# Performance work log

Measured on AMD Instinct MI355X. Metric: run time of the kernel, lower is better.

Reference implementation:

```python
import jax, jax.numpy as jnp
import numpy as np

N_NODES = 100000

def setup_inputs() -> dict:
    key = jax.random.key(0)
    k1, k2, k3, k4, k5 = jax.random.split(key, 5)
    E = 1600000
    feat = jax.random.normal(k1, (N_NODES, 128), dtype=jnp.float32)
    W = jax.random.normal(k2, (128, 32), dtype=jnp.float32) * 0.08  # ~xavier scale
    edge_w = jax.random.uniform(k3, (E,), dtype=jnp.float32)
    src = jax.random.randint(k4, (E,), 0, N_NODES, dtype=jnp.int32)
    dst = jax.random.randint(k5, (E,), 0, N_NODES, dtype=jnp.int32)
    return {"feat": feat, "W": W, "edge_w": edge_w, "src": src, "dst": dst}

def reference(feat, W, edge_w, src, dst):
    # linear transform: [N, in] @ [in, out] -> [N, out]
    h = feat @ W
    # gather source features per edge, scale by edge weight: u_mul_e
    m = h[src] * edge_w[:, None]  # [E, out]
    # sum messages at destination nodes
    rst = jax.ops.segment_sum(m, dst, num_segments=N_NODES)  # [N, out]
    return rst
```

## Files before the change

### kernel.cpp

```cpp
#include <hip/hip_runtime.h>
#include <hip/hip_fp16.h>

constexpr int N_IN    = 128;
constexpr int N_OUT   = 32;
constexpr int LOG_R   = 6;
constexpr int RANGE   = 1 << LOG_R;
constexpr int MAXNB   = 2048;
constexpr int NCC     = 256;
constexpr int PBLK    = 512;
constexpr int CHUNK_P = 2048;

union H4 { uint2 u; __half2 h2[2]; };

__global__ __launch_bounds__(256) void gemm_h(
    const float* __restrict__ feat, const float* __restrict__ W,
    __half* __restrict__ h, int n)
{
    __shared__ float Ws[N_IN * N_OUT];
    for (int i = threadIdx.x; i < (N_IN * N_OUT) / 4; i += 256)
        reinterpret_cast<float4*>(Ws)[i] = reinterpret_cast<const float4*>(W)[i];
    __syncthreads();

    int gid = blockIdx.x * 256 + threadIdx.x;
    int row = gid >> 3;
    if (row >= n) return;
    int cg = (gid & 7) * 4;

    const float4* frow = reinterpret_cast<const float4*>(feat + (size_t)row * N_IN);
    float4 acc = make_float4(0.f, 0.f, 0.f, 0.f);
    #pragma unroll
    for (int k4 = 0; k4 < N_IN / 4; ++k4) {
        float4 f = frow[k4];
        int k = k4 * 4;
        float4 w0 = *reinterpret_cast<const float4*>(&Ws[(k + 0) * N_OUT + cg]);
        float4 w1 = *reinterpret_cast<const float4*>(&Ws[(k + 1) * N_OUT + cg]);
        float4 w2 = *reinterpret_cast<const float4*>(&Ws[(k + 2) * N_OUT + cg]);
        float4 w3 = *reinterpret_cast<const float4*>(&Ws[(k + 3) * N_OUT + cg]);
        acc.x += f.x * w0.x + f.y * w1.x + f.z * w2.x + f.w * w3.x;
        acc.y += f.x * w0.y + f.y * w1.y + f.z * w2.y + f.w * w3.y;
        acc.z += f.x * w0.z + f.y * w1.z + f.z * w2.z + f.w * w3.z;
        acc.w += f.x * w0.w + f.y * w1.w + f.z * w2.w + f.w * w3.w;
    }
    H4 v;
    v.h2[0] = __float22half2_rn(make_float2(acc.x, acc.y));
    v.h2[1] = __float22half2_rn(make_float2(acc.z, acc.w));
    *reinterpret_cast<uint2*>(h + (size_t)row * N_OUT + cg) = v.u;
}

__global__ __launch_bounds__(PBLK) void partition2_k(
    const int* __restrict__ src, const int* __restrict__ dst,
    const float* __restrict__ w, int* __restrict__ tbl,
    int2* __restrict__ sw, int E, int NB, int epc)
{
    __shared__ int hist[MAXNB];
    __shared__ int wscan[PBLK];

    const int c   = blockIdx.x;
    const int tid = threadIdx.x;
    const int e0  = c * epc;
    const int e1  = min(e0 + epc, E);
    const int m   = max(e1 - e0, 0);
    const int m4  = m & ~3;
    const int slots = (NB + PBLK - 1) / PBLK;

    for (int i = tid; i < NB; i += PBLK) hist[i] = 0;
    __syncthreads();

    for (int o = tid * 4; o < m4; o += PBLK * 4) {
        int4 dv = *reinterpret_cast<const int4*>(dst + e0 + o);
        atomicAdd(&hist[dv.x >> LOG_R], 1);
        atomicAdd(&hist[dv.y >> LOG_R], 1);
        atomicAdd(&hist[dv.z >> LOG_R], 1);
        atomicAdd(&hist[dv.w >> LOG_R], 1);
    }
    if (m4 + tid < m) atomicAdd(&hist[dst[e0 + m4 + tid] >> LOG_R], 1);
    __syncthreads();

    int tsum = 0;
    int base = tid * slots;
    for (int j = 0; j < slots; ++j) {
        int idx = base + j;
        if (idx < NB) tsum += hist[idx];
    }
    wscan[tid] = tsum;
    __syncthreads();
    for (int off = 1; off < PBLK; off <<= 1) {
        int x = (tid >= off) ? wscan[tid - off] : 0;
        __syncthreads();
        wscan[tid] += x;
        __syncthreads();
    }
    int run = wscan[tid] - tsum;
    __syncthreads();
    for (int j = 0; j < slots; ++j) {
        int idx = base + j;
        if (idx < NB) {
            int cval = hist[idx];
            tbl[(size_t)c * (NB + 1) + idx] = run;
            hist[idx] = run;
            run += cval;
        }
    }
    if (tid == 0) tbl[(size_t)c * (NB + 1) + NB] = m;
    __syncthreads();

    int2* outp = sw + (size_t)c * epc;
    for (int o = tid * 4; o < m4; o += PBLK * 4) {
        int4   sv = *reinterpret_cast<const int4*>(src + e0 + o);
        int4   dv = *reinterpret_cast<const int4*>(dst + e0 + o);
        float4 wv = *reinterpret_cast<const float4*>(w + e0 + o);
        int p0 = atomicAdd(&hist[dv.x >> LOG_R], 1);
        int p1 = atomicAdd(&hist[dv.y >> LOG_R], 1);
        int p2 = atomicAdd(&hist[dv.z >> LOG_R], 1);
        int p3 = atomicAdd(&hist[dv.w >> LOG_R], 1);
        outp[p0] = make_int2(sv.x | ((dv.x & (RANGE - 1)) << 17), __float_as_int(wv.x));
        outp[p1] = make_int2(sv.y | ((dv.y & (RANGE - 1)) << 17), __float_as_int(wv.y));
        outp[p2] = make_int2(sv.z | ((dv.z & (RANGE - 1)) << 17), __float_as_int(wv.z));
        outp[p3] = make_int2(sv.w | ((dv.w & (RANGE - 1)) << 17), __float_as_int(wv.w));
    }
    if (m4 + tid < m) {
        int e = e0 + m4 + tid;
        int d = dst[e];
        int pos = atomicAdd(&hist[d >> LOG_R], 1);
        outp[pos] = make_int2(src[e] | ((d & (RANGE - 1)) << 17), __float_as_int(w[e]));
    }
}

__global__ __launch_bounds__(256) void conv4_k(
    const __half* __restrict__ h, const int2* __restrict__ sw,
    const int* __restrict__ tbl, float* __restrict__ out,
    int n, int NB, int ncc, int epc)
{
    __shared__ int2 pairs[CHUNK_P];
    __shared__ int2 pairs_s[CHUNK_P];
    __shared__ int cnt[RANGE];
    __shared__ int sc[RANGE];
    __shared__ int start[RANGE + 1];
    __shared__ int cur[RANGE];
    __shared__ int rs[NCC];
    __shared__ int ps[NCC + 1];
    __shared__ int stmp[256];

    const int b   = blockIdx.x;
    const int tid = threadIdx.x;
    const int g   = tid >> 3;
    const int cg  = (tid & 7) * 4;

    int len = 0;
    if (tid < ncc) {
        int s0 = tbl[(size_t)tid * (NB + 1) + b];
        int s1 = tbl[(size_t)tid * (NB + 1) + b + 1];
        rs[tid] = s0;
        len = s1 - s0;
    }
    stmp[tid] = len;
    __syncthreads();
    for (int off = 1; off < 256; off <<= 1) {
        int x = (tid >= off) ? stmp[tid - off] : 0;
        __syncthreads();
        stmp[tid] += x;
        __syncthreads();
    }
    ps[tid + 1] = stmp[tid];
    if (tid == 0) ps[0] = 0;
    __syncthreads();
    const int deg = ps[ncc];

    float4 accA = make_float4(0.f, 0.f, 0.f, 0.f);
    float4 accB = make_float4(0.f, 0.f, 0.f, 0.f);

    #define LOAD_H(p, f01, f23)                                                \
        H4 _u##f01;                                                            \
        _u##f01.u = *reinterpret_cast<const uint2*>(                           \
            h + (size_t)((p).x & 0x1FFFF) * N_OUT + cg);                       \
        float2 f01 = __half22float2(_u##f01.h2[0]);                            \
        float2 f23 = __half22float2(_u##f01.h2[1]);
    #define ACC_STEP(p, f01, f23)                                              \
    {                                                                          \
        float wv  = __int_as_float((p).y);                                     \
        int   odd = ((p).x >> 17) & 1;                                         \
        float wa = odd ? 0.f : wv, wb = odd ? wv : 0.f;                        \
        accA.x += f01.x * wa; accA.y += f01.y * wa;                            \
        accA.z += f23.x * wa; accA.w += f23.y * wa;                            \
        accB.x += f01.x * wb; accB.y += f01.y * wb;                            \
        accB.z += f23.x * wb; accB.w += f23.y * wb;                            \
    }

    if (deg <= CHUNK_P) {
        if (tid < RANGE) cnt[tid] = 0;
        __syncthreads();

        if (tid < ncc) {
            int d0 = ps[tid];
            int l  = ps[tid + 1] - d0;
            const int2* sp = sw + (size_t)tid * epc + rs[tid];
            for (int j = 0; j < l; ++j) {
                int2 p = sp[j];
                pairs[d0 + j] = p;
                atomicAdd(&cnt[p.x >> 17], 1);
            }
        }
        __syncthreads();

        int v = 0;
        if (tid < RANGE) { v = cnt[tid]; sc[tid] = v; }
        __syncthreads();
        #pragma unroll
        for (int off = 1; off < RANGE; off <<= 1) {
            int x = (tid < RANGE && tid >= off) ? sc[tid - off] : 0;
            __syncthreads();
            if (tid < RANGE) sc[tid] += x;
            __syncthreads();
        }
        if (tid < RANGE) { start[tid] = sc[tid] - v; cur[tid] = sc[tid] - v; }
        if (tid == RANGE - 1) start[RANGE] = sc[RANGE - 1];
        __syncthreads();

        for (int i = tid; i < deg; i += 256) {
            int2 p = pairs[i];
            int pos = atomicAdd(&cur[p.x >> 17], 1);
            pairs_s[pos] = p;
        }
        __syncthreads();

        int k  = start[2 * g];
        int ke = start[2 * g + 2];
        for (; k + 3 < ke; k += 4) {
            int2 p0 = pairs_s[k + 0], p1 = pairs_s[k + 1];
            int2 p2 = pairs_s[k + 2], p3 = pairs_s[k + 3];
            LOAD_H(p0, a01, a23)
            LOAD_H(p1, b01, b23)
            LOAD_H(p2, c01, c23)
            LOAD_H(p3, d01, d23)
            ACC_STEP(p0, a01, a23)
            ACC_STEP(p1, b01, b23)
            ACC_STEP(p2, c01, c23)
            ACC_STEP(p3, d01, d23)
        }
        for (; k < ke; ++k) {
            int2 p = pairs_s[k];
            LOAD_H(p, e01, e23)
            ACC_STEP(p, e01, e23)
        }
    } else {
        for (int cbase = 0; cbase < deg; cbase += CHUNK_P) {
            const int m = min(CHUNK_P, deg - cbase);

            for (int i = tid; i < m; i += 256) {
                int gidx = cbase + i;
                int lo = 0, hi = ncc - 1;
                while (lo < hi) {
                    int mid = (lo + hi + 1) >> 1;
                    if (ps[mid] <= gidx) lo = mid; else hi = mid - 1;
                }
                int off = gidx - ps[lo];
                pairs[i] = sw[(size_t)lo * epc + rs[lo] + off];
            }
            if (tid < RANGE) cnt[tid] = 0;
            __syncthreads();

            for (int i = tid; i < m; i += 256)
                atomicAdd(&cnt[pairs[i].x >> 17], 1);
            __syncthreads();

            int v = 0;
            if (tid < RANGE) { v = cnt[tid]; sc[tid] = v; }
            __syncthreads();
            #pragma unroll
            for (int off = 1; off < RANGE; off <<= 1) {
                int x = (tid < RANGE && tid >= off) ? sc[tid - off] : 0;
                __syncthreads();
                if (tid < RANGE) sc[tid] += x;
                __syncthreads();
            }
            if (tid < RANGE) { start[tid] = sc[tid] - v; cur[tid] = sc[tid] - v; }
            if (tid == RANGE - 1) start[RANGE] = sc[RANGE - 1];
            __syncthreads();

            for (int i = tid; i < m; i += 256) {
                int2 p = pairs[i];
                int pos = atomicAdd(&cur[p.x >> 17], 1);
                pairs_s[pos] = p;
            }
            __syncthreads();

            int k  = start[2 * g];
            int ke = start[2 * g + 2];
            for (; k < ke; ++k) {
                int2 p = pairs_s[k];
                LOAD_H(p, f01, f23)
                ACC_STEP(p, f01, f23)
            }
            __syncthreads();
        }
    }
    #undef LOAD_H
    #undef ACC_STEP

    const int lo2 = b * RANGE;
    int node0 = lo2 + 2 * g;
    if (node0 < n)
        *reinterpret_cast<float4*>(out + (size_t)node0 * N_OUT + cg) = accA;
    if (node0 + 1 < n)
        *reinterpret_cast<float4*>(out + (size_t)(node0 + 1) * N_OUT + cg) = accB;
}

__global__ __launch_bounds__(256) void fused_edge(
    const float* __restrict__ feat, const float* __restrict__ W,
    const float* __restrict__ edge_w, const int* __restrict__ src,
    const int* __restrict__ dst, float* __restrict__ out, int E)
{
    __shared__ float Ws[N_IN * N_OUT];
    for (int i = threadIdx.x; i < (N_IN * N_OUT) / 4; i += 256)
        reinterpret_cast<float4*>(Ws)[i] = reinterpret_cast<const float4*>(W)[i];
    __syncthreads();
    int gid = blockIdx.x * 256 + threadIdx.x;
    int e = gid >> 3;
    if (e >= E) return;
    int cg = (gid & 7) * 4;
    int s = src[e];
    int d = dst[e];
    float w = edge_w[e];
    const float4* frow = reinterpret_cast<const float4*>(feat + (size_t)s * N_IN);
    float4 acc = make_float4(0.f, 0.f, 0.f, 0.f);
    #pragma unroll
    for (int k4 = 0; k4 < N_IN / 4; ++k4) {
        float4 f = frow[k4];
        int k = k4 * 4;
        float4 w0 = *reinterpret_cast<const float4*>(&Ws[(k + 0) * N_OUT + cg]);
        float4 w1 = *reinterpret_cast<const float4*>(&Ws[(k + 1) * N_OUT + cg]);
        float4 w2 = *reinterpret_cast<const float4*>(&Ws[(k + 2) * N_OUT + cg]);
        float4 w3 = *reinterpret_cast<const float4*>(&Ws[(k + 3) * N_OUT + cg]);
        acc.x += f.x * w0.x + f.y * w1.x + f.z * w2.x + f.w * w3.x;
        acc.y += f.x * w0.y + f.y * w1.y + f.z * w2.y + f.w * w3.y;
        acc.z += f.x * w0.z + f.y * w1.z + f.z * w2.z + f.w * w3.z;
        acc.w += f.x * w0.w + f.y * w1.w + f.z * w2.w + f.w * w3.w;
    }
    float* o = out + (size_t)d * N_OUT + cg;
    atomicAdd(o + 0, acc.x * w);
    atomicAdd(o + 1, acc.y * w);
    atomicAdd(o + 2, acc.z * w);
    atomicAdd(o + 3, acc.w * w);
}

extern "C" void kernel_launch(void* const* d_in, const int* in_sizes, int n_in,
                              void* d_out, int out_size, void* d_ws, size_t ws_size,
                              hipStream_t stream) {
    const float* feat   = (const float*)d_in[0];
    const float* W      = (const float*)d_in[1];
    const float* edge_w = (const float*)d_in[2];
    const int*   src    = (const int*)d_in[3];
    const int*   dst    = (const int*)d_in[4];
    float* out = (float*)d_out;

    int n = in_sizes[0] / N_IN;
    int E = in_sizes[2];

    int NB  = (n + RANGE - 1) / RANGE;
    int ncc = NCC;
    int epc = (((E + ncc - 1) / ncc) + 3) & ~3;

    size_t off_h   = 0;
    size_t off_tbl = (off_h + (size_t)n * N_OUT * sizeof(__half) + 15) & ~(size_t)15;
    size_t off_sw  = (off_tbl + (size_t)ncc * (NB + 1) * sizeof(int) + 15) & ~(size_t)15;
    size_t need    = off_sw + (size_t)ncc * epc * sizeof(int2);

    bool ok = (ws_size >= need) && (n <= (1 << 17)) && (NB <= MAXNB);

    if (ok) {
        char* ws = (char*)d_ws;
        __half* h  = (__half*)(ws + off_h);
        int*   tbl = (int*)(ws + off_tbl);
        int2*  sw  = (int2*)(ws + off_sw);

        long gthreads = (long)n * 8;
        gemm_h<<<(int)((gthreads + 255) / 256), 256, 0, stream>>>(feat, W, h, n);
        partition2_k<<<ncc, PBLK, 0, stream>>>(src, dst, edge_w, tbl, sw, E, NB, epc);
        conv4_k<<<NB, 256, 0, stream>>>(h, sw, tbl, out, n, NB, ncc, epc);
    } else {
        hipError_t _e = hipMemsetAsync(d_out, 0, (size_t)out_size * sizeof(float), stream);
        (void)_e;
        long sthreads = (long)E * 8;
        fused_edge<<<(int)((sthreads + 255) / 256), 256, 0, stream>>>(feat, W, edge_w, src, dst, out, E);
    }
}
```

Before: 78.65 us.

## Map four threads per node with 16-byte gathers and drop staging buffer

The aggregation kernel now gives each destination node four threads, each loading eight half values with one 16-byte load. Previously eight threads handled a pair of nodes and masked the weight to zero for the non-matching node. The intermediate shared pairs buffer is removed: each thread reads its chunk directly from global memory twice, once to histogram and once to scatter. The overflow path now has every thread scan the whole chunk and keep only its own node's edges, replacing the sort. This removes the wasted multiply-adds and a shared-memory copy, at the cost of re-reading global pairs and a slower fallback for high-degree blocks.

```diff
diff --git a/kernel.cpp b/kernel.cpp
--- a/kernel.cpp
+++ b/kernel.cpp
@@ -11,6 +11,7 @@
 constexpr int CHUNK_P = 2048;
 
 union H4 { uint2 u; __half2 h2[2]; };
+union H8 { uint4 u; __half2 h2[4]; };
 
 __global__ __launch_bounds__(256) void gemm_h(
     const float* __restrict__ feat, const float* __restrict__ W,
@@ -126,12 +127,11 @@
     }
 }
 
-__global__ __launch_bounds__(256) void conv4_k(
+__global__ __launch_bounds__(256) void conv5_k(
     const __half* __restrict__ h, const int2* __restrict__ sw,
     const int* __restrict__ tbl, float* __restrict__ out,
     int n, int NB, int ncc, int epc)
 {
-    __shared__ int2 pairs[CHUNK_P];
     __shared__ int2 pairs_s[CHUNK_P];
     __shared__ int cnt[RANGE];
     __shared__ int sc[RANGE];
@@ -141,10 +141,10 @@
     __shared__ int ps[NCC + 1];
     __shared__ int stmp[256];
 
-    const int b   = blockIdx.x;
-    const int tid = threadIdx.x;
-    const int g   = tid >> 3;
-    const int cg  = (tid & 7) * 4;
+    const int b    = blockIdx.x;
+    const int tid  = threadIdx.x;
+    const int node = tid >> 2;
+    const int cg8  = (tid & 3) * 8;
 
     int len = 0;
     if (tid < ncc) {
@@ -166,40 +166,35 @@
     __syncthreads();
     const int deg = ps[ncc];
 
-    float4 accA = make_float4(0.f, 0.f, 0.f, 0.f);
-    float4 accB = make_float4(0.f, 0.f, 0.f, 0.f);
-
-    #define LOAD_H(p, f01, f23)                                                \
-        H4 _u##f01;                                                            \
-        _u##f01.u = *reinterpret_cast<const uint2*>(                           \
-            h + (size_t)((p).x & 0x1FFFF) * N_OUT + cg);                       \
-        float2 f01 = __half22float2(_u##f01.h2[0]);                            \
-        float2 f23 = __half22float2(_u##f01.h2[1]);
-    #define ACC_STEP(p, f01, f23)                                              \
+    float4 acc01 = make_float4(0.f, 0.f, 0.f, 0.f);
+    float4 acc23 = make_float4(0.f, 0.f, 0.f, 0.f);
+
+    #define GLOAD(p, f0, f1, f2, f3)                                           \
+        H8 _x##f0;                                                             \
+        _x##f0.u = *reinterpret_cast<const uint4*>(                            \
+            h + (size_t)((p).x & 0x1FFFF) * N_OUT + cg8);                      \
+        float2 f0 = __half22float2(_x##f0.h2[0]);                              \
+        float2 f1 = __half22float2(_x##f0.h2[1]);                              \
+        float2 f2 = __half22float2(_x##f0.h2[2]);                              \
+        float2 f3 = __half22float2(_x##f0.h2[3]);
+    #define GACC(p, f0, f1, f2, f3)                                            \
     {                                                                          \
-        float wv  = __int_as_float((p).y);                                     \
-        int   odd = ((p).x >> 17) & 1;                                         \
-        float wa = odd ? 0.f : wv, wb = odd ? wv : 0.f;                        \
-        accA.x += f01.x * wa; accA.y += f01.y * wa;                            \
-        accA.z += f23.x * wa; accA.w += f23.y * wa;                            \
-        accB.x += f01.x * wb; accB.y += f01.y * wb;                            \
-        accB.z += f23.x * wb; accB.w += f23.y * wb;                            \
+        float wv = __int_as_float((p).y);                                      \
+        acc01.x += f0.x * wv; acc01.y += f0.y * wv;                            \
+        acc01.z += f1.x * wv; acc01.w += f1.y * wv;                            \
+        acc23.x += f2.x * wv; acc23.y += f2.y * wv;                            \
+        acc23.z += f3.x * wv; acc23.w += f3.y * wv;                            \
     }
 
     if (deg <= CHUNK_P) {
-        if (tid < RANGE) cnt[tid] = 0;
-        __syncthreads();
-
-        if (tid < ncc) {
-            int d0 = ps[tid];
-            int l  = ps[tid + 1] - d0;
-            const int2* sp = sw + (size_t)tid * epc + rs[tid];
-            for (int j = 0; j < l; ++j) {
-                int2 p = sp[j];
-                pairs[d0 + j] = p;
-                atomicAdd(&cnt[p.x >> 17], 1);
-            }
-        }
+        if (tid < RANGE) { cnt[tid] = 0; }
+        __syncthreads();
+
+        const int2* sp = sw + (size_t)tid * epc + rs[tid];
+        const int   l  = ps[tid + 1] - ps[tid];
+
+        for (int j = 0; j < l; ++j)
+            atomicAdd(&cnt[sp[j].x >> 17], 1);
         __syncthreads();
 
         int v = 0;
@@ -216,36 +211,35 @@
         if (tid == RANGE - 1) start[RANGE] = sc[RANGE - 1];
         __syncthreads();
 
-        for (int i = tid; i < deg; i += 256) {
-            int2 p = pairs[i];
+        for (int j = 0; j < l; ++j) {
+            int2 p = sp[j];
             int pos = atomicAdd(&cur[p.x >> 17], 1);
             pairs_s[pos] = p;
         }
         __syncthreads();
 
-        int k  = start[2 * g];
-        int ke = start[2 * g + 2];
+        int k  = start[node];
+        int ke = start[node + 1];
         for (; k + 3 < ke; k += 4) {
             int2 p0 = pairs_s[k + 0], p1 = pairs_s[k + 1];
             int2 p2 = pairs_s[k + 2], p3 = pairs_s[k + 3];
-            LOAD_H(p0, a01, a23)
-            LOAD_H(p1, b01, b23)
-            LOAD_H(p2, c01, c23)
-            LOAD_H(p3, d01, d23)
-            ACC_STEP(p0, a01, a23)
-            ACC_STEP(p1, b01, b23)
-            ACC_STEP(p2, c01, c23)
-            ACC_STEP(p3, d01, d23)
+            GLOAD(p0, a0, a1, a2, a3)
+            GLOAD(p1, b0, b1, b2, b3)
+            GLOAD(p2, c0, c1, c2, c3)
+            GLOAD(p3, d0, d1, d2, d3)
+            GACC(p0, a0, a1, a2, a3)
+            GACC(p1, b0, b1, b2, b3)
+            GACC(p2, c0, c1, c2, c3)
+            GACC(p3, d0, d1, d2, d3)
         }
         for (; k < ke; ++k) {
             int2 p = pairs_s[k];
-            LOAD_H(p, e01, e23)
-            ACC_STEP(p, e01, e23)
+            GLOAD(p, e0, e1, e2, e3)
+            GACC(p, e0, e1, e2, e3)
         }
     } else {
         for (int cbase = 0; cbase < deg; cbase += CHUNK_P) {
             const int m = min(CHUNK_P, deg - cbase);
-
             for (int i = tid; i < m; i += 256) {
                 int gidx = cbase + i;
                 int lo = 0, hi = ncc - 1;
@@ -254,55 +248,28 @@
                     if (ps[mid] <= gidx) lo = mid; else hi = mid - 1;
                 }
                 int off = gidx - ps[lo];
-                pairs[i] = sw[(size_t)lo * epc + rs[lo] + off];
-            }
-            if (tid < RANGE) cnt[tid] = 0;
-            __syncthreads();
-
-            for (int i = tid; i < m; i += 256)
-                atomicAdd(&cnt[pairs[i].x >> 17], 1);
-            __syncthreads();
-
-            int v = 0;
-            if (tid < RANGE) { v = cnt[tid]; sc[tid] = v; }
-            __syncthreads();
-            #pragma unroll
-            for (int off = 1; off < RANGE; off <<= 1) {
-                int x = (tid < RANGE && tid >= off) ? sc[tid - off] : 0;
-                __syncthreads();
-                if (tid < RANGE) sc[tid] += x;
-                __syncthreads();
-            }
-            if (tid < RANGE) { start[tid] = sc[tid] - v; cur[tid] = sc[tid] - v; }
-            if (tid == RANGE - 1) start[RANGE] = sc[RANGE - 1];
-            __syncthreads();
-
-            for (int i = tid; i < m; i += 256) {
-                int2 p = pairs[i];
-                int pos = atomicAdd(&cur[p.x >> 17], 1);
-                pairs_s[pos] = p;
+                pairs_s[i] = sw[(size_t)lo * epc + rs[lo] + off];
             }
             __syncthreads();
-
-            int k  = start[2 * g];
-            int ke = start[2 * g + 2];
-            for (; k < ke; ++k) {
+            for (int k = 0; k < m; ++k) {
                 int2 p = pairs_s[k];
-                LOAD_H(p, f01, f23)
-                ACC_STEP(p, f01, f23)
+                if ((p.x >> 17) == node) {
+                    GLOAD(p, f0, f1, f2, f3)
+                    GACC(p, f0, f1, f2, f3)
+                }
             }
             __syncthreads();
         }
     }
-    #undef LOAD_H
-    #undef ACC_STEP
-
-    const int lo2 = b * RANGE;
-    int node0 = lo2 + 2 * g;
-    if (node0 < n)
-        *reinterpret_cast<float4*>(out + (size_t)node0 * N_OUT + cg) = accA;
-    if (node0 + 1 < n)
-        *reinterpret_cast<float4*>(out + (size_t)(node0 + 1) * N_OUT + cg) = accB;
+    #undef GLOAD
+    #undef GACC
+
+    int node0 = b * RANGE + node;
+    if (node0 < n) {
+        float* o = out + (size_t)node0 * N_OUT + cg8;
+        *reinterpret_cast<float4*>(o + 0) = acc01;
+        *reinterpret_cast<float4*>(o + 4) = acc23;
+    }
 }
 
 __global__ __launch_bounds__(256) void fused_edge(
@@ -376,7 +343,7 @@
         long gthreads = (long)n * 8;
         gemm_h<<<(int)((gthreads + 255) / 256), 256, 0, stream>>>(feat, W, h, n);
         partition2_k<<<ncc, PBLK, 0, stream>>>(src, dst, edge_w, tbl, sw, E, NB, epc);
-        conv4_k<<<NB, 256, 0, stream>>>(h, sw, tbl, out, n, NB, ncc, epc);
+        conv5_k<<<NB, 256, 0, stream>>>(h, sw, tbl, out, n, NB, ncc, epc);
     } else {
         hipError_t _e = hipMemsetAsync(d_out, 0, (size_t)out_size * sizeof(float), stream);
         (void)_e;
```

New measurement: 84.33 us. +7.2%, slower.
